# Performance work log

Measured on AMD Instinct MI355X. Metric: run time of the kernel, lower is better.

## Reference

```python
import jax, jax.numpy as jnp
import numpy as np

N, T, CUT = 64, 2, 25.0            # atoms, atom types, cutoff radius
ED = [3, 32, 64, 128]              # embedding MLP dims (input 3)
LD = [384, 256, 256, 128, 3]       # per-atom MLP dims (input 3*E)
P = T * (T + 1) // 2               # number of unordered type pairs
M = 27 * N                         # periodic images


def setup_inputs() -> dict:
    key = jax.random.key(0)
    ks = jax.random.split(key, 16)
    x = jax.random.uniform(ks[0], (N, 3), jnp.float32) * 10.0
    lattice = 10.0 * jnp.eye(3, dtype=jnp.float32)
    atom_types = (jnp.arange(N) % T).astype(jnp.int32)

    def lin(k, shape, fan_in):
        return jax.random.normal(k, shape, jnp.float32) / np.sqrt(fan_in)

    inp = {"x": x, "lattice": lattice}
    for i in range(3):
        inp[f"We{i+1}"] = lin(ks[1 + i], (P, ED[i], ED[i + 1]), ED[i])
        inp[f"be{i+1}"] = jnp.zeros((P, ED[i + 1]), jnp.float32)
    for i in range(4):
        inp[f"Wl{i+1}"] = lin(ks[5 + i], (N, LD[i], LD[i + 1]), LD[i])
        inp[f"bl{i+1}"] = jnp.zeros((N, LD[i + 1]), jnp.float32)
    inp["atom_types"] = atom_types
    return inp


def reference(x, lattice, We1, be1, We2, be2, We3, be3,
              Wl1, bl1, Wl2, bl2, Wl3, bl3, Wl4, bl4, atom_types):
    act = jax.nn.leaky_relu  # slope 0.01, matches nn.LeakyReLU default
    idx = jnp.arange(-1, 2, dtype=x.dtype)
    # (i,j,k) combos in the same loop order as torch (i slowest, k fastest)
    combos = jnp.stack(jnp.meshgrid(idx, idx, idx, indexing="ij"), -1).reshape(27, 3)
    x_ext = (x[None, :, :] + (combos @ lattice)[:, None, :]).reshape(M, 3)  # [M,3]
    # the in-place subtraction in torch telescopes: at step n, x_ext = x_ext0 - x_ext0[n]
    rel = x_ext[None, :, :] - x_ext[:N, None, :]                    # [N,M,3]
    dist = jnp.linalg.norm(rel, axis=-1)                            # [N,M]
    mask = dist <= CUT
    rank = jnp.cumsum(mask, axis=1) - 1
    # torch removes POSITION n of the compacted neighbor list -> rank == n
    keep = (mask & (rank != jnp.arange(N)[:, None])).astype(x.dtype)  # [N,M]

    types_ext = jnp.tile(atom_types, 27)                            # [M]
    lo = jnp.minimum(atom_types[:, None], types_ext[None, :])
    hi = jnp.maximum(atom_types[:, None], types_ext[None, :])
    pid = lo * T - (lo * (lo - 1)) // 2 + (hi - lo)                 # [N,M] pair-type id

    # run all P pair-type embedding MLPs on every candidate edge, then route
    h = act(jnp.einsum("nmi,pio->pnmo", rel, We1) + be1[:, None, None, :])
    h = act(jnp.einsum("pnmi,pio->pnmo", h, We2) + be2[:, None, None, :])
    h = act(jnp.einsum("pnmi,pio->pnmo", h, We3) + be3[:, None, None, :])
    g = h[pid, jnp.arange(N)[:, None], jnp.arange(M)[None, :], :]   # [N,M,E]

    # d_n = g_n^T @ x_n over kept neighbors; row-major flatten of [E,3] -> [3E]
    d = jnp.einsum("nm,nme,nmc->nec", keep, g, rel).reshape(N, -1)  # [N,3E]

    h = act(jnp.einsum("ni,nio->no", d, Wl1) + bl1)
    h = act(jnp.einsum("ni,nio->no", h, Wl2) + bl2)
    h = act(jnp.einsum("ni,nio->no", h, Wl3) + bl3)
    out = jnp.einsum("ni,nio->no", h, Wl4) + bl4                    # [N,3]
    out = out - jnp.mean(out, axis=0, keepdims=True)
    return out.reshape(-1)                                          # [3N]
```

## Files before the change

### kernel.cpp

```cpp
#include <hip/hip_runtime.h>

#define LEAKY(t) ((t) > 0.0f ? (t) : 0.01f*(t))

typedef __attribute__((ext_vector_type(8))) short short8;
typedef __attribute__((ext_vector_type(4))) float floatx4;

static __device__ __forceinline__ short f2bf(float f) {
  unsigned u = __float_as_uint(f);
  u += 0x7FFFu + ((u >> 16) & 1u);
  return (short)(u >> 16);
}

__global__ __launch_bounds__(256) void embed_kernel(
    const float* __restrict__ x, const float* __restrict__ lattice,
    const float* __restrict__ We1, const float* __restrict__ be1,
    const float* __restrict__ We2, const float* __restrict__ be2,
    const float* __restrict__ We3, const float* __restrict__ be3,
    const int* __restrict__ types, float* __restrict__ dpt)
{
  __shared__ __align__(16) unsigned char smem[59392];
  float* W1f = (float*)smem;
  float* b2f = (float*)(smem + 512);
  float* b3f = (float*)(smem + 768);
  short* W2T = (short*)(smem + 1280);
  short* W3T = (short*)(smem + 6400);
  short* h1s = (short*)(smem + 24832);
  short* h2s = (short*)(smem + 36352);
  float* rk4 = (float*)(smem + 57088);

  const int n = blockIdx.x, par = blockIdx.y, chunk = blockIdx.z;
  const int tid = threadIdx.x;

  const int tn = types[n];
  const int tj = types[par];
  const int lo = tn < tj ? tn : tj;
  const int hi = tn < tj ? tj : tn;
  const int p  = lo * 2 - (lo * (lo - 1)) / 2 + (hi - lo);

  if (tid < 96)  W1f[tid] = We1[p*96 + tid];
  if (tid >= 96 && tid < 128) W1f[tid] = be1[p*32 + tid - 96];
  if (tid < 64)  b2f[tid] = be2[p*64 + tid];
  if (tid < 128) b3f[tid] = be3[p*128 + tid];
  for (int idx = tid; idx < 2048; idx += 256) {
    const int i = idx >> 6, o = idx & 63;
    W2T[o*40 + i] = f2bf(We2[p*2048 + idx]);
  }
  for (int idx = tid; idx < 8192; idx += 256) {
    const int i = idx >> 7, o = idx & 127;
    W3T[o*72 + i] = f2bf(We3[p*8192 + idx]);
  }
  __syncthreads();

  if (tid < 144) {
    const int q  = chunk*144 + tid;
    const int c  = q >> 5;
    const int jj = q & 31;
    const int j  = 2*jj + par;
    const float f0 = (float)(c / 9);
    const float f1 = (float)((c / 3) % 3);
    const float f2c = (float)(c % 3);
    const float rel0 = x[j*3+0] - x[n*3+0] + f0*lattice[0] + f1*lattice[3] + f2c*lattice[6];
    const float rel1 = x[j*3+1] - x[n*3+1] + f0*lattice[1] + f1*lattice[4] + f2c*lattice[7];
    const float rel2 = x[j*3+2] - x[n*3+2] + f0*lattice[2] + f1*lattice[5] + f2c*lattice[8];
    const float dist2 = rel0*rel0 + rel1*rel1 + rel2*rel2;
    const int m = c*64 + j;
    const bool keep = (dist2 <= 625.0f) && (m != n);
    const float kf = keep ? 1.0f : 0.0f;
    rk4[tid*4+0] = rel0*kf; rk4[tid*4+1] = rel1*kf;
    rk4[tid*4+2] = rel2*kf; rk4[tid*4+3] = 0.0f;
    #pragma unroll
    for (int o = 0; o < 32; ++o) {
      float v = rel0*W1f[o] + rel1*W1f[32+o] + rel2*W1f[64+o] + W1f[96+o];
      h1s[tid*40 + o] = f2bf(LEAKY(v));
    }
  }
  __syncthreads();

  const int lane = tid & 63, w = tid >> 6;
  const int col = lane & 15, quad = lane >> 4;

  {
    const short8 bfrag = *(const short8*)&W2T[(w*16+col)*40 + quad*8];
    const float bias2 = b2f[w*16+col];
    #pragma unroll
    for (int m = 0; m < 9; ++m) {
      const short8 a = *(const short8*)&h1s[(m*16+col)*40 + quad*8];
      floatx4 acc = {bias2, bias2, bias2, bias2};
      acc = __builtin_amdgcn_mfma_f32_16x16x32_bf16(a, bfrag, acc, 0, 0, 0);
      #pragma unroll
      for (int r = 0; r < 4; ++r) {
        const int pair = m*16 + quad*4 + r;
        h2s[pair*72 + w*16 + col] = f2bf(LEAKY(acc[r]));
      }
    }
  }
  __syncthreads();

  {
    short8 bfrag[2][2];
    float bias3[2];
    #pragma unroll
    for (int nt = 0; nt < 2; ++nt) {
      bias3[nt] = b3f[w*32 + nt*16 + col];
      #pragma unroll
      for (int ks = 0; ks < 2; ++ks)
        bfrag[nt][ks] = *(const short8*)&W3T[(w*32 + nt*16 + col)*72 + ks*32 + quad*8];
    }
    float vacc[2][3] = {{0,0,0},{0,0,0}};
    #pragma unroll
    for (int m = 0; m < 9; ++m) {
      const short8 a0 = *(const short8*)&h2s[(m*16+col)*72 +  0 + quad*8];
      const short8 a1 = *(const short8*)&h2s[(m*16+col)*72 + 32 + quad*8];
      float4 rks[4];
      #pragma unroll
      for (int r = 0; r < 4; ++r)
        rks[r] = *(const float4*)&rk4[(m*16 + quad*4 + r)*4];
      #pragma unroll
      for (int nt = 0; nt < 2; ++nt) {
        floatx4 acc = {bias3[nt], bias3[nt], bias3[nt], bias3[nt]};
        acc = __builtin_amdgcn_mfma_f32_16x16x32_bf16(a0, bfrag[nt][0], acc, 0, 0, 0);
        acc = __builtin_amdgcn_mfma_f32_16x16x32_bf16(a1, bfrag[nt][1], acc, 0, 0, 0);
        #pragma unroll
        for (int r = 0; r < 4; ++r) {
          const float h3 = LEAKY(acc[r]);
          vacc[nt][0] += h3 * rks[r].x;
          vacc[nt][1] += h3 * rks[r].y;
          vacc[nt][2] += h3 * rks[r].z;
        }
      }
    }
    #pragma unroll
    for (int nt = 0; nt < 2; ++nt)
      #pragma unroll
      for (int c = 0; c < 3; ++c) {
        float v = vacc[nt][c];
        v += __shfl_xor(v, 16, 64);
        v += __shfl_xor(v, 32, 64);
        vacc[nt][c] = v;
      }
    if (lane < 32) {
      const int nts = lane >> 4, colw = lane & 15;
      const int o = w*32 + nts*16 + colw;
      #pragma unroll
      for (int c = 0; c < 3; ++c) {
        const float val = nts ? vacc[1][c] : vacc[0][c];
        atomicAdd(&dpt[n*384 + o*3 + c], val);
      }
    }
  }
}

__global__ __launch_bounds__(256) void fit1_kernel(
    const float* __restrict__ d, const float* __restrict__ W,
    const float* __restrict__ b, float* __restrict__ out)
{
  __shared__ float din[384];
  __shared__ floatx4 red[256];
  const int n = blockIdx.x, slice = blockIdx.y, tid = threadIdx.x;
  for (int i = tid; i < 384; i += 256) din[i] = d[n*384 + i];
  __syncthreads();
  const int g = tid & 15, s = tid >> 4;
  const int os = slice*64;
  const float* Wp = W + (size_t)n*98304 + os + 4*g;
  floatx4 acc = {0,0,0,0};
  #pragma unroll 6
  for (int k = 0; k < 24; ++k) {
    const int i = s*24 + k;
    const floatx4 w4 = *(const floatx4*)(Wp + (size_t)i*256);
    acc += din[i] * w4;
  }
  red[tid] = acc;
  __syncthreads();
  #pragma unroll
  for (int off = 128; off >= 16; off >>= 1) {
    if (tid < off) red[tid] += red[tid + off];
    __syncthreads();
  }
  if (tid < 16) {
    const floatx4 v = red[tid];
    const int o = os + 4*tid;
    const float4 bb = *(const float4*)&b[n*256 + o];
    float4 r;
    r.x = LEAKY(v[0] + bb.x); r.y = LEAKY(v[1] + bb.y);
    r.z = LEAKY(v[2] + bb.z); r.w = LEAKY(v[3] + bb.w);
    *(float4*)&out[n*256 + o] = r;
  }
}

__global__ __launch_bounds__(256) void fit2_kernel(
    const float* __restrict__ in, const float* __restrict__ W,
    const float* __restrict__ b, float* __restrict__ out)
{
  __shared__ float din[256];
  __shared__ floatx4 red[256];
  const int n = blockIdx.x, slice = blockIdx.y, tid = threadIdx.x;
  din[tid] = in[n*256 + tid];
  __syncthreads();
  const int g = tid & 15, s = tid >> 4;
  const int os = slice*64;
  const float* Wp = W + (size_t)n*65536 + os + 4*g;
  floatx4 acc = {0,0,0,0};
  #pragma unroll 8
  for (int k = 0; k < 16; ++k) {
    const int i = s*16 + k;
    const floatx4 w4 = *(const floatx4*)(Wp + (size_t)i*256);
    acc += din[i] * w4;
  }
  red[tid] = acc;
  __syncthreads();
  #pragma unroll
  for (int off = 128; off >= 16; off >>= 1) {
    if (tid < off) red[tid] += red[tid + off];
    __syncthreads();
  }
  if (tid < 16) {
    const floatx4 v = red[tid];
    const int o = os + 4*tid;
    const float4 bb = *(const float4*)&b[n*256 + o];
    float4 r;
    r.x = LEAKY(v[0] + bb.x); r.y = LEAKY(v[1] + bb.y);
    r.z = LEAKY(v[2] + bb.z); r.w = LEAKY(v[3] + bb.w);
    *(float4*)&out[n*256 + o] = r;
  }
}

__global__ __launch_bounds__(256) void fit3_kernel(
    const float* __restrict__ in, const float* __restrict__ W,
    const float* __restrict__ b, float* __restrict__ out)
{
  __shared__ float din[256];
  __shared__ floatx4 red[256];
  const int n = blockIdx.x, slice = blockIdx.y, tid = threadIdx.x;
  din[tid] = in[n*256 + tid];
  __syncthreads();
  const int g = tid & 7, s = tid >> 3;
  const int os = slice*32;
  const float* Wp = W + (size_t)n*32768 + os + 4*g;
  floatx4 acc = {0,0,0,0};
  #pragma unroll 8
  for (int k = 0; k < 8; ++k) {
    const int i = s*8 + k;
    const floatx4 w4 = *(const floatx4*)(Wp + (size_t)i*128);
    acc += din[i] * w4;
  }
  red[tid] = acc;
  __syncthreads();
  #pragma unroll
  for (int off = 128; off >= 8; off >>= 1) {
    if (tid < off) red[tid] += red[tid + off];
    __syncthreads();
  }
  if (tid < 8) {
    const floatx4 v = red[tid];
    const int o = os + 4*tid;
    const float4 bb = *(const float4*)&b[n*128 + o];
    float4 r;
    r.x = LEAKY(v[0] + bb.x); r.y = LEAKY(v[1] + bb.y);
    r.z = LEAKY(v[2] + bb.z); r.w = LEAKY(v[3] + bb.w);
    *(float4*)&out[n*128 + o] = r;
  }
}

__global__ __launch_bounds__(256) void fit4_kernel(
    const float* __restrict__ h3, const float* __restrict__ W,
    const float* __restrict__ b, float* __restrict__ out)
{
  __shared__ float part[256 * 3];
  __shared__ float pre[192];
  __shared__ float meanv[3];
  const int tid = threadIdx.x;
  const int n = tid >> 2, q = tid & 3;
  const float* Wn = W + (size_t)n * 384;
  const float* h  = h3 + n * 128;
  float a0 = 0.f, a1 = 0.f, a2 = 0.f;
  for (int k = 0; k < 32; ++k) {
    const int i = q * 32 + k;
    const float hv = h[i];
    a0 += hv * Wn[i*3 + 0];
    a1 += hv * Wn[i*3 + 1];
    a2 += hv * Wn[i*3 + 2];
  }
  part[tid*3+0] = a0; part[tid*3+1] = a1; part[tid*3+2] = a2;
  __syncthreads();
  if (tid < 192) {
    const int nn = tid / 3, o = tid % 3;
    float t = part[(nn*4+0)*3+o] + part[(nn*4+1)*3+o]
            + part[(nn*4+2)*3+o] + part[(nn*4+3)*3+o] + b[tid];
    pre[tid] = t;
  }
  __syncthreads();
  if (tid < 3) {
    float s = 0.f;
    for (int nn = 0; nn < 64; ++nn) s += pre[nn*3 + tid];
    meanv[tid] = s * (1.0f / 64.0f);
  }
  __syncthreads();
  if (tid < 192) out[tid] = pre[tid] - meanv[tid % 3];
}

extern "C" void kernel_launch(void* const* d_in, const int* in_sizes, int n_in,
                              void* d_out, int out_size, void* d_ws, size_t ws_size,
                              hipStream_t stream) {
  const float* x       = (const float*)d_in[0];
  const float* lattice = (const float*)d_in[1];
  const float* We1 = (const float*)d_in[2];
  const float* be1 = (const float*)d_in[3];
  const float* We2 = (const float*)d_in[4];
  const float* be2 = (const float*)d_in[5];
  const float* We3 = (const float*)d_in[6];
  const float* be3 = (const float*)d_in[7];
  const float* Wl1 = (const float*)d_in[8];
  const float* bl1 = (const float*)d_in[9];
  const float* Wl2 = (const float*)d_in[10];
  const float* bl2 = (const float*)d_in[11];
  const float* Wl3 = (const float*)d_in[12];
  const float* bl3 = (const float*)d_in[13];
  const float* Wl4 = (const float*)d_in[14];
  const float* bl4 = (const float*)d_in[15];
  const int*   types = (const int*)d_in[16];

  float* w   = (float*)d_ws;
  float* dpt = w;
  float* h1f = w + 24576;
  float* h2f = h1f + 16384;
  float* h3f = h2f + 16384;

  hipMemsetAsync(dpt, 0, 64*384*sizeof(float), stream);
  embed_kernel<<<dim3(64, 2, 6), 256, 0, stream>>>(
      x, lattice, We1, be1, We2, be2, We3, be3, types, dpt);
  fit1_kernel<<<dim3(64, 4), 256, 0, stream>>>(dpt, Wl1, bl1, h1f);
  fit2_kernel<<<dim3(64, 4), 256, 0, stream>>>(h1f, Wl2, bl2, h2f);
  fit3_kernel<<<dim3(64, 4), 256, 0, stream>>>(h2f, Wl3, bl3, h3f);
  fit4_kernel<<<1, 256, 0, stream>>>(h3f, Wl4, bl4, (float*)d_out);
}
```

Measured before the change: 150.7 us.

## Pre-transpose embedding weights, drop atomics, fuse fitting layers 2-4

A new prep kernel converts and transposes the embedding weights to bf16 once per call, so each embed block copies them with vector loads instead of transposing them itself. The embed output goes to per-block partial slots that fit1 sums, which removes the memset and the atomic adds. The layer-1 activation is computed from interleaved float4 weights and stored as packed short8. Fit layers 2-4 and the mean subtraction are merged into one kernel that uses a last-block counter, cutting three launches. In exchange the fused fit kernel runs on only 64 blocks, and it adds an extra launch plus more workspace.

```diff
diff --git a/kernel.cpp b/kernel.cpp
--- a/kernel.cpp
+++ b/kernel.cpp
@@ -11,15 +11,38 @@
   return (short)(u >> 16);
 }
 
+
+__global__ __launch_bounds__(256) void prep_kernel(
+    const float* __restrict__ We1, const float* __restrict__ be1,
+    const float* __restrict__ We2, const float* __restrict__ We3,
+    float* __restrict__ g_W1v, short* __restrict__ g_WT,
+    unsigned int* __restrict__ cnt)
+{
+  const int gt = blockIdx.x * 256 + threadIdx.x;
+  const int GS = gridDim.x * 256;
+  if (gt == 0) *cnt = 0;
+  for (int idx = gt; idx < 3 * 128; idx += GS) {
+    const int p = idx >> 7, r = idx & 127, o = r >> 2, c = r & 3;
+    g_W1v[idx] = (c < 3) ? We1[p * 96 + c * 32 + o] : be1[p * 32 + o];
+  }
+  for (int idx = gt; idx < 3 * 2560; idx += GS) {
+    const int p = idx / 2560, r = idx % 2560, o = r / 40, i = r % 40;
+    g_WT[p * 11776 + o * 40 + i] = (i < 32) ? f2bf(We2[p * 2048 + i * 64 + o]) : (short)0;
+  }
+  for (int idx = gt; idx < 3 * 9216; idx += GS) {
+    const int p = idx / 9216, r = idx % 9216, o = r / 72, i = r % 72;
+    g_WT[p * 11776 + 2560 + o * 72 + i] = (i < 64) ? f2bf(We3[p * 8192 + i * 128 + o]) : (short)0;
+  }
+}
+
 __global__ __launch_bounds__(256) void embed_kernel(
     const float* __restrict__ x, const float* __restrict__ lattice,
-    const float* __restrict__ We1, const float* __restrict__ be1,
-    const float* __restrict__ We2, const float* __restrict__ be2,
-    const float* __restrict__ We3, const float* __restrict__ be3,
+    const float* __restrict__ g_W1v, const short* __restrict__ g_WT,
+    const float* __restrict__ be2, const float* __restrict__ be3,
     const int* __restrict__ types, float* __restrict__ dpt)
 {
   __shared__ __align__(16) unsigned char smem[59392];
-  float* W1f = (float*)smem;
+  float* W1v = (float*)smem;
   float* b2f = (float*)(smem + 512);
   float* b3f = (float*)(smem + 768);
   short* W2T = (short*)(smem + 1280);
@@ -37,25 +60,25 @@
   const int hi = tn < tj ? tj : tn;
   const int p  = lo * 2 - (lo * (lo - 1)) / 2 + (hi - lo);
 
-  if (tid < 96)  W1f[tid] = We1[p*96 + tid];
-  if (tid >= 96 && tid < 128) W1f[tid] = be1[p*32 + tid - 96];
-  if (tid < 64)  b2f[tid] = be2[p*64 + tid];
-  if (tid < 128) b3f[tid] = be3[p*128 + tid];
-  for (int idx = tid; idx < 2048; idx += 256) {
-    const int i = idx >> 6, o = idx & 63;
-    W2T[o*40 + i] = f2bf(We2[p*2048 + idx]);
-  }
-  for (int idx = tid; idx < 8192; idx += 256) {
-    const int i = idx >> 7, o = idx & 127;
-    W3T[o*72 + i] = f2bf(We3[p*8192 + idx]);
+  if (tid < 32) ((float4*)W1v)[tid] = ((const float4*)(g_W1v + p * 128))[tid];
+  if (tid < 64)  b2f[tid] = be2[p * 64 + tid];
+  if (tid < 128) b3f[tid] = be3[p * 128 + tid];
+  {
+    const short8* src = (const short8*)(g_WT + p * 11776);
+    short8* dst = (short8*)W2T;
+    #pragma unroll
+    for (int k = 0; k < 6; ++k) {
+      const int idx = tid + k * 256;
+      if (idx < 1472) dst[idx] = src[idx];
+    }
   }
   __syncthreads();
 
   if (tid < 144) {
-    const int q  = chunk*144 + tid;
+    const int q  = chunk * 144 + tid;
     const int c  = q >> 5;
     const int jj = q & 31;
-    const int j  = 2*jj + par;
+    const int j  = 2 * jj + par;
     const float f0 = (float)(c / 9);
     const float f1 = (float)((c / 3) % 3);
     const float f2c = (float)(c % 3);
@@ -63,15 +86,22 @@
     const float rel1 = x[j*3+1] - x[n*3+1] + f0*lattice[1] + f1*lattice[4] + f2c*lattice[7];
     const float rel2 = x[j*3+2] - x[n*3+2] + f0*lattice[2] + f1*lattice[5] + f2c*lattice[8];
     const float dist2 = rel0*rel0 + rel1*rel1 + rel2*rel2;
-    const int m = c*64 + j;
+    const int m = c * 64 + j;
     const bool keep = (dist2 <= 625.0f) && (m != n);
     const float kf = keep ? 1.0f : 0.0f;
     rk4[tid*4+0] = rel0*kf; rk4[tid*4+1] = rel1*kf;
     rk4[tid*4+2] = rel2*kf; rk4[tid*4+3] = 0.0f;
-    #pragma unroll
-    for (int o = 0; o < 32; ++o) {
-      float v = rel0*W1f[o] + rel1*W1f[32+o] + rel2*W1f[64+o] + W1f[96+o];
-      h1s[tid*40 + o] = f2bf(LEAKY(v));
+    const float4* W1v4 = (const float4*)W1v;
+    #pragma unroll
+    for (int g = 0; g < 4; ++g) {
+      short8 pk;
+      #pragma unroll
+      for (int u = 0; u < 8; ++u) {
+        const float4 wv = W1v4[g*8 + u];
+        const float v = rel0*wv.x + rel1*wv.y + rel2*wv.z + wv.w;
+        pk[u] = f2bf(LEAKY(v));
+      }
+      *(short8*)&h1s[tid*40 + g*8] = pk;
     }
   }
   __syncthreads();
@@ -141,33 +171,37 @@
     if (lane < 32) {
       const int nts = lane >> 4, colw = lane & 15;
       const int o = w*32 + nts*16 + colw;
-      #pragma unroll
-      for (int c = 0; c < 3; ++c) {
-        const float val = nts ? vacc[1][c] : vacc[0][c];
-        atomicAdd(&dpt[n*384 + o*3 + c], val);
-      }
+      float* dst = dpt + ((size_t)(n*12) + par*6 + chunk) * 384 + o*3;
+      dst[0] = nts ? vacc[1][0] : vacc[0][0];
+      dst[1] = nts ? vacc[1][1] : vacc[0][1];
+      dst[2] = nts ? vacc[1][2] : vacc[0][2];
     }
   }
 }
 
 __global__ __launch_bounds__(256) void fit1_kernel(
-    const float* __restrict__ d, const float* __restrict__ W,
+    const float* __restrict__ dpt, const float* __restrict__ W,
     const float* __restrict__ b, float* __restrict__ out)
 {
   __shared__ float din[384];
   __shared__ floatx4 red[256];
   const int n = blockIdx.x, slice = blockIdx.y, tid = threadIdx.x;
-  for (int i = tid; i < 384; i += 256) din[i] = d[n*384 + i];
+  for (int i = tid; i < 384; i += 256) {
+    const float* dp = dpt + (size_t)n * 4608 + i;
+    float s = 0.f;
+    #pragma unroll
+    for (int k = 0; k < 12; ++k) s += dp[k * 384];
+    din[i] = s;
+  }
   __syncthreads();
   const int g = tid & 15, s = tid >> 4;
-  const int os = slice*64;
-  const float* Wp = W + (size_t)n*98304 + os + 4*g;
-  floatx4 acc = {0,0,0,0};
+  const int os = slice * 64;
+  const float* Wp = W + (size_t)n * 98304 + os + 4 * g;
+  floatx4 acc = {0, 0, 0, 0};
   #pragma unroll 6
   for (int k = 0; k < 24; ++k) {
-    const int i = s*24 + k;
-    const floatx4 w4 = *(const floatx4*)(Wp + (size_t)i*256);
-    acc += din[i] * w4;
+    const int i = s * 24 + k;
+    acc += din[i] * *(const floatx4*)(Wp + (size_t)i * 256);
   }
   red[tid] = acc;
   __syncthreads();
@@ -178,124 +212,121 @@
   }
   if (tid < 16) {
     const floatx4 v = red[tid];
-    const int o = os + 4*tid;
-    const float4 bb = *(const float4*)&b[n*256 + o];
+    const int o = os + 4 * tid;
+    const float4 bb = *(const float4*)&b[n * 256 + o];
     float4 r;
     r.x = LEAKY(v[0] + bb.x); r.y = LEAKY(v[1] + bb.y);
     r.z = LEAKY(v[2] + bb.z); r.w = LEAKY(v[3] + bb.w);
-    *(float4*)&out[n*256 + o] = r;
-  }
-}
-
-__global__ __launch_bounds__(256) void fit2_kernel(
-    const float* __restrict__ in, const float* __restrict__ W,
-    const float* __restrict__ b, float* __restrict__ out)
+    *(float4*)&out[n * 256 + o] = r;
+  }
+}
+
+__global__ __launch_bounds__(512) void fit234_kernel(
+    const float* __restrict__ h1f,
+    const float* __restrict__ Wl2, const float* __restrict__ bl2,
+    const float* __restrict__ Wl3, const float* __restrict__ bl3,
+    const float* __restrict__ Wl4, const float* __restrict__ bl4,
+    float* __restrict__ pre_g, unsigned int* __restrict__ cnt,
+    float* __restrict__ out)
 {
-  __shared__ float din[256];
-  __shared__ floatx4 red[256];
-  const int n = blockIdx.x, slice = blockIdx.y, tid = threadIdx.x;
-  din[tid] = in[n*256 + tid];
-  __syncthreads();
-  const int g = tid & 15, s = tid >> 4;
-  const int os = slice*64;
-  const float* Wp = W + (size_t)n*65536 + os + 4*g;
-  floatx4 acc = {0,0,0,0};
-  #pragma unroll 8
-  for (int k = 0; k < 16; ++k) {
-    const int i = s*16 + k;
-    const floatx4 w4 = *(const floatx4*)(Wp + (size_t)i*256);
-    acc += din[i] * w4;
-  }
-  red[tid] = acc;
+  __shared__ float h[256];
+  __shared__ floatx4 red[512];
+  __shared__ float h3s[128];
+  __shared__ float pre_s[192];
+  __shared__ int amlast;
+  const int n = blockIdx.x, tid = threadIdx.x;
+
+  if (tid < 256) h[tid] = h1f[n * 256 + tid];
+  __syncthreads();
+
+  {
+    const int o4 = tid & 63, s = tid >> 6;
+    const float* Wp = Wl2 + (size_t)n * 65536 + 4 * o4;
+    floatx4 acc = {0, 0, 0, 0};
+    #pragma unroll 8
+    for (int k = 0; k < 32; ++k) {
+      const int i = s * 32 + k;
+      acc += h[i] * *(const floatx4*)(Wp + (size_t)i * 256);
+    }
+    red[tid] = acc;
+  }
+  __syncthreads();
+  if (tid < 64) {
+    floatx4 a = red[tid];
+    #pragma unroll
+    for (int s = 1; s < 8; ++s) a += red[tid + s * 64];
+    const float4 bb = *(const float4*)&bl2[n * 256 + 4 * tid];
+    h[4*tid+0] = LEAKY(a[0] + bb.x);
+    h[4*tid+1] = LEAKY(a[1] + bb.y);
+    h[4*tid+2] = LEAKY(a[2] + bb.z);
+    h[4*tid+3] = LEAKY(a[3] + bb.w);
+  }
+  __syncthreads();
+
+  {
+    const int o4 = tid & 31, s = tid >> 5;
+    const float* Wp = Wl3 + (size_t)n * 32768 + 4 * o4;
+    floatx4 acc = {0, 0, 0, 0};
+    #pragma unroll 8
+    for (int k = 0; k < 16; ++k) {
+      const int i = s * 16 + k;
+      acc += h[i] * *(const floatx4*)(Wp + (size_t)i * 128);
+    }
+    red[tid] = acc;
+  }
+  __syncthreads();
+  if (tid < 32) {
+    floatx4 a = red[tid];
+    #pragma unroll
+    for (int s = 1; s < 16; ++s) a += red[tid + s * 32];
+    const float4 bb = *(const float4*)&bl3[n * 128 + 4 * tid];
+    h3s[4*tid+0] = LEAKY(a[0] + bb.x);
+    h3s[4*tid+1] = LEAKY(a[1] + bb.y);
+    h3s[4*tid+2] = LEAKY(a[2] + bb.z);
+    h3s[4*tid+3] = LEAKY(a[3] + bb.w);
+  }
+  __syncthreads();
+
+  if (tid < 128) {
+    const float hv = h3s[tid];
+    floatx4 v;
+    v[0] = hv * Wl4[(size_t)n * 384 + tid * 3 + 0];
+    v[1] = hv * Wl4[(size_t)n * 384 + tid * 3 + 1];
+    v[2] = hv * Wl4[(size_t)n * 384 + tid * 3 + 2];
+    v[3] = 0.f;
+    red[tid] = v;
+  }
   __syncthreads();
   #pragma unroll
-  for (int off = 128; off >= 16; off >>= 1) {
+  for (int off = 64; off >= 1; off >>= 1) {
     if (tid < off) red[tid] += red[tid + off];
     __syncthreads();
   }
-  if (tid < 16) {
-    const floatx4 v = red[tid];
-    const int o = os + 4*tid;
-    const float4 bb = *(const float4*)&b[n*256 + o];
-    float4 r;
-    r.x = LEAKY(v[0] + bb.x); r.y = LEAKY(v[1] + bb.y);
-    r.z = LEAKY(v[2] + bb.z); r.w = LEAKY(v[3] + bb.w);
-    *(float4*)&out[n*256 + o] = r;
-  }
-}
-
-__global__ __launch_bounds__(256) void fit3_kernel(
-    const float* __restrict__ in, const float* __restrict__ W,
-    const float* __restrict__ b, float* __restrict__ out)
-{
-  __shared__ float din[256];
-  __shared__ floatx4 red[256];
-  const int n = blockIdx.x, slice = blockIdx.y, tid = threadIdx.x;
-  din[tid] = in[n*256 + tid];
-  __syncthreads();
-  const int g = tid & 7, s = tid >> 3;
-  const int os = slice*32;
-  const float* Wp = W + (size_t)n*32768 + os + 4*g;
-  floatx4 acc = {0,0,0,0};
-  #pragma unroll 8
-  for (int k = 0; k < 8; ++k) {
-    const int i = s*8 + k;
-    const floatx4 w4 = *(const floatx4*)(Wp + (size_t)i*128);
-    acc += din[i] * w4;
-  }
-  red[tid] = acc;
-  __syncthreads();
-  #pragma unroll
-  for (int off = 128; off >= 8; off >>= 1) {
-    if (tid < off) red[tid] += red[tid + off];
+  if (tid < 3) {
+    const float pre = red[0][tid] + bl4[n * 3 + tid];
+    __hip_atomic_store(&pre_g[n * 3 + tid], pre, __ATOMIC_RELAXED,
+                       __HIP_MEMORY_SCOPE_AGENT);
+  }
+  __threadfence();
+  if (tid == 0) {
+    const unsigned old = __hip_atomic_fetch_add(cnt, 1u, __ATOMIC_ACQ_REL,
+                                                __HIP_MEMORY_SCOPE_AGENT);
+    amlast = (old == 63u);
+  }
+  __syncthreads();
+  if (amlast) {
+    if (tid < 192)
+      pre_s[tid] = __hip_atomic_load(&pre_g[tid], __ATOMIC_RELAXED,
+                                     __HIP_MEMORY_SCOPE_AGENT);
     __syncthreads();
-  }
-  if (tid < 8) {
-    const floatx4 v = red[tid];
-    const int o = os + 4*tid;
-    const float4 bb = *(const float4*)&b[n*128 + o];
-    float4 r;
-    r.x = LEAKY(v[0] + bb.x); r.y = LEAKY(v[1] + bb.y);
-    r.z = LEAKY(v[2] + bb.z); r.w = LEAKY(v[3] + bb.w);
-    *(float4*)&out[n*128 + o] = r;
-  }
-}
-
-__global__ __launch_bounds__(256) void fit4_kernel(
-    const float* __restrict__ h3, const float* __restrict__ W,
-    const float* __restrict__ b, float* __restrict__ out)
-{
-  __shared__ float part[256 * 3];
-  __shared__ float pre[192];
-  __shared__ float meanv[3];
-  const int tid = threadIdx.x;
-  const int n = tid >> 2, q = tid & 3;
-  const float* Wn = W + (size_t)n * 384;
-  const float* h  = h3 + n * 128;
-  float a0 = 0.f, a1 = 0.f, a2 = 0.f;
-  for (int k = 0; k < 32; ++k) {
-    const int i = q * 32 + k;
-    const float hv = h[i];
-    a0 += hv * Wn[i*3 + 0];
-    a1 += hv * Wn[i*3 + 1];
-    a2 += hv * Wn[i*3 + 2];
-  }
-  part[tid*3+0] = a0; part[tid*3+1] = a1; part[tid*3+2] = a2;
-  __syncthreads();
-  if (tid < 192) {
-    const int nn = tid / 3, o = tid % 3;
-    float t = part[(nn*4+0)*3+o] + part[(nn*4+1)*3+o]
-            + part[(nn*4+2)*3+o] + part[(nn*4+3)*3+o] + b[tid];
-    pre[tid] = t;
-  }
-  __syncthreads();
-  if (tid < 3) {
-    float s = 0.f;
-    for (int nn = 0; nn < 64; ++nn) s += pre[nn*3 + tid];
-    meanv[tid] = s * (1.0f / 64.0f);
-  }
-  __syncthreads();
-  if (tid < 192) out[tid] = pre[tid] - meanv[tid % 3];
+    if (tid < 3) {
+      float s = 0.f;
+      for (int nn = 0; nn < 64; ++nn) s += pre_s[nn * 3 + tid];
+      h3s[tid] = s * (1.0f / 64.0f);
+    }
+    __syncthreads();
+    if (tid < 192) out[tid] = pre_s[tid] - h3s[tid % 3];
+  }
 }
 
 extern "C" void kernel_launch(void* const* d_in, const int* in_sizes, int n_in,
@@ -319,17 +350,18 @@
   const float* bl4 = (const float*)d_in[15];
   const int*   types = (const int*)d_in[16];
 
-  float* w   = (float*)d_ws;
-  float* dpt = w;
-  float* h1f = w + 24576;
-  float* h2f = h1f + 16384;
-  float* h3f = h2f + 16384;
-
-  hipMemsetAsync(dpt, 0, 64*384*sizeof(float), stream);
+  float* wsf = (float*)d_ws;
+  float*        dpt   = wsf;
+  float*        h1f   = wsf + 294912;
+  float*        pre_g = wsf + 311296;
+  unsigned int* cnt   = (unsigned int*)(wsf + 311488);
+  float*        g_W1v = wsf + 311492;
+  short*        g_WT  = (short*)(wsf + 311876);
+
+  prep_kernel<<<64, 256, 0, stream>>>(We1, be1, We2, We3, g_W1v, g_WT, cnt);
   embed_kernel<<<dim3(64, 2, 6), 256, 0, stream>>>(
-      x, lattice, We1, be1, We2, be2, We3, be3, types, dpt);
+      x, lattice, g_W1v, g_WT, be2, be3, types, dpt);
   fit1_kernel<<<dim3(64, 4), 256, 0, stream>>>(dpt, Wl1, bl1, h1f);
-  fit2_kernel<<<dim3(64, 4), 256, 0, stream>>>(h1f, Wl2, bl2, h2f);
-  fit3_kernel<<<dim3(64, 4), 256, 0, stream>>>(h2f, Wl3, bl3, h3f);
-  fit4_kernel<<<1, 256, 0, stream>>>(h3f, Wl4, bl4, (float*)d_out);
-}
+  fit234_kernel<<<64, 512, 0, stream>>>(h1f, Wl2, bl2, Wl3, bl3, Wl4, bl4,
+                                        pre_g, cnt, (float*)d_out);
+}
```

After: 147.2 us. -2.3%, faster.

## Prepack embedding weights, MFMA first layer, fuse fit3/fit4, widen fit grids

Applied to the files above, without the earlier changes.

A new prep kernel converts the embedding weights to bf16 in MFMA fragment order once and also zeroes the accumulator and a counter, which replaces the memset. The embed kernel then loads weight fragments straight into registers instead of transposing them into LDS in every block, and computes layer 1 with MFMA. The fit kernels run on twice as many blocks with smaller output slices. fit3 and fit4 are merged through a last-block-done atomic counter, removing one launch at the cost of fence and atomic overhead.

```diff
diff --git a/kernel.cpp b/kernel.cpp
--- a/kernel.cpp
+++ b/kernel.cpp
@@ -11,25 +11,72 @@
   return (short)(u >> 16);
 }
 
-__global__ __launch_bounds__(256) void embed_kernel(
+
+__global__ __launch_bounds__(256) void prep_kernel(
+    const float* __restrict__ We1, const float* __restrict__ be1,
+    const float* __restrict__ We2, const float* __restrict__ We3,
+    short* __restrict__ g_WT, float* __restrict__ d,
+    unsigned int* __restrict__ cnt)
+{
+  const int gt = blockIdx.x * 256 + threadIdx.x;
+  const int GS = gridDim.x * 256;
+  if (gt == 0) *cnt = 0;
+  for (int i = gt; i < 6144; i += GS) {
+    const float4 z = {0.f, 0.f, 0.f, 0.f};
+    ((float4*)d)[i] = z;
+  }
+  for (int it = gt; it < 4224; it += GS) {
+    short8 v;
+    if (it < 384) {
+      const int p = it >> 7, r = it & 127, ot = (r >> 6) & 1, ln = r & 63;
+      const int col = ln & 15, quad = ln >> 4, o = ot * 16 + col;
+      #pragma unroll
+      for (int j = 0; j < 8; ++j) {
+        const int k = quad * 8 + j;
+        float f = 0.0f;
+        if (k < 3) f = We1[p * 96 + k * 32 + o];
+        else if (k == 3) f = be1[p * 32 + o];
+        v[j] = f2bf(f);
+      }
+    } else if (it < 1152) {
+      const int t = it - 384;
+      const int p = t >> 8, r = t & 255, ot = r >> 6, ln = r & 63;
+      const int col = ln & 15, quad = ln >> 4, o = ot * 16 + col;
+      #pragma unroll
+      for (int j = 0; j < 8; ++j) {
+        const int k = quad * 8 + j;
+        v[j] = f2bf(We2[p * 2048 + k * 64 + o]);
+      }
+    } else {
+      const int t = it - 1152;
+      const int p = t >> 10, r = t & 1023, ot = r >> 7, rr = r & 127;
+      const int ks = rr >> 6, ln = rr & 63;
+      const int col = ln & 15, quad = ln >> 4, o = ot * 16 + col;
+      #pragma unroll
+      for (int j = 0; j < 8; ++j) {
+        const int k = ks * 32 + quad * 8 + j;
+        v[j] = f2bf(We3[p * 8192 + k * 128 + o]);
+      }
+    }
+    *(short8*)(g_WT + it * 8) = v;
+  }
+}
+
+__global__ __launch_bounds__(256, 4) void embed_kernel(
     const float* __restrict__ x, const float* __restrict__ lattice,
-    const float* __restrict__ We1, const float* __restrict__ be1,
-    const float* __restrict__ We2, const float* __restrict__ be2,
-    const float* __restrict__ We3, const float* __restrict__ be3,
-    const int* __restrict__ types, float* __restrict__ dpt)
-{
-  __shared__ __align__(16) unsigned char smem[59392];
-  float* W1f = (float*)smem;
-  float* b2f = (float*)(smem + 512);
-  float* b3f = (float*)(smem + 768);
-  short* W2T = (short*)(smem + 1280);
-  short* W3T = (short*)(smem + 6400);
-  short* h1s = (short*)(smem + 24832);
-  short* h2s = (short*)(smem + 36352);
-  float* rk4 = (float*)(smem + 57088);
+    const short* __restrict__ g_WT,
+    const float* __restrict__ be2, const float* __restrict__ be3,
+    const int* __restrict__ types, float* __restrict__ d)
+{
+  __shared__ __align__(16) float rel4[144 * 4];
+  __shared__ __align__(16) float rk4[144 * 4];
+  __shared__ __align__(16) short h1s[144 * 40];
+  __shared__ __align__(16) short h2s[144 * 72];
 
   const int n = blockIdx.x, par = blockIdx.y, chunk = blockIdx.z;
   const int tid = threadIdx.x;
+  const int lane = tid & 63, w = tid >> 6;
+  const int col = lane & 15, quad = lane >> 4;
 
   const int tn = types[n];
   const int tj = types[par];
@@ -37,25 +84,30 @@
   const int hi = tn < tj ? tj : tn;
   const int p  = lo * 2 - (lo * (lo - 1)) / 2 + (hi - lo);
 
-  if (tid < 96)  W1f[tid] = We1[p*96 + tid];
-  if (tid >= 96 && tid < 128) W1f[tid] = be1[p*32 + tid - 96];
-  if (tid < 64)  b2f[tid] = be2[p*64 + tid];
-  if (tid < 128) b3f[tid] = be3[p*128 + tid];
-  for (int idx = tid; idx < 2048; idx += 256) {
-    const int i = idx >> 6, o = idx & 63;
-    W2T[o*40 + i] = f2bf(We2[p*2048 + idx]);
-  }
-  for (int idx = tid; idx < 8192; idx += 256) {
-    const int i = idx >> 7, o = idx & 127;
-    W3T[o*72 + i] = f2bf(We3[p*8192 + idx]);
-  }
-  __syncthreads();
+  const short8* WT8 = (const short8*)g_WT;
+  const short8 w1b0 = WT8[(p * 2 + 0) * 64 + lane];
+  const short8 w1b1 = WT8[(p * 2 + 1) * 64 + lane];
+  short8 w2b[4];
+  #pragma unroll
+  for (int ot = 0; ot < 4; ++ot) w2b[ot] = WT8[384 + (p * 4 + ot) * 64 + lane];
+  short8 w3b[2][2];
+  #pragma unroll
+  for (int nt = 0; nt < 2; ++nt)
+    #pragma unroll
+    for (int ks = 0; ks < 2; ++ks)
+      w3b[nt][ks] = WT8[1152 + ((p * 8 + 2 * w + nt) * 2 + ks) * 64 + lane];
+  float bias2[4];
+  #pragma unroll
+  for (int ot = 0; ot < 4; ++ot) bias2[ot] = be2[p * 64 + ot * 16 + col];
+  float bias3[2];
+  #pragma unroll
+  for (int nt = 0; nt < 2; ++nt) bias3[nt] = be3[p * 128 + w * 32 + nt * 16 + col];
 
   if (tid < 144) {
-    const int q  = chunk*144 + tid;
+    const int q  = chunk * 144 + tid;
     const int c  = q >> 5;
     const int jj = q & 31;
-    const int j  = 2*jj + par;
+    const int j  = 2 * jj + par;
     const float f0 = (float)(c / 9);
     const float f1 = (float)((c / 3) % 3);
     const float f2c = (float)(c % 3);
@@ -63,90 +115,87 @@
     const float rel1 = x[j*3+1] - x[n*3+1] + f0*lattice[1] + f1*lattice[4] + f2c*lattice[7];
     const float rel2 = x[j*3+2] - x[n*3+2] + f0*lattice[2] + f1*lattice[5] + f2c*lattice[8];
     const float dist2 = rel0*rel0 + rel1*rel1 + rel2*rel2;
-    const int m = c*64 + j;
+    const int m = c * 64 + j;
     const bool keep = (dist2 <= 625.0f) && (m != n);
     const float kf = keep ? 1.0f : 0.0f;
+    rel4[tid*4+0] = rel0; rel4[tid*4+1] = rel1;
+    rel4[tid*4+2] = rel2; rel4[tid*4+3] = 1.0f;
     rk4[tid*4+0] = rel0*kf; rk4[tid*4+1] = rel1*kf;
     rk4[tid*4+2] = rel2*kf; rk4[tid*4+3] = 0.0f;
-    #pragma unroll
-    for (int o = 0; o < 32; ++o) {
-      float v = rel0*W1f[o] + rel1*W1f[32+o] + rel2*W1f[64+o] + W1f[96+o];
-      h1s[tid*40 + o] = f2bf(LEAKY(v));
-    }
-  }
-  __syncthreads();
-
-  const int lane = tid & 63, w = tid >> 6;
-  const int col = lane & 15, quad = lane >> 4;
-
-  {
-    const short8 bfrag = *(const short8*)&W2T[(w*16+col)*40 + quad*8];
-    const float bias2 = b2f[w*16+col];
-    #pragma unroll
-    for (int m = 0; m < 9; ++m) {
-      const short8 a = *(const short8*)&h1s[(m*16+col)*40 + quad*8];
-      floatx4 acc = {bias2, bias2, bias2, bias2};
-      acc = __builtin_amdgcn_mfma_f32_16x16x32_bf16(a, bfrag, acc, 0, 0, 0);
+  }
+  __syncthreads();
+
+  for (int mt = w; mt < 9; mt += 4) {
+    const float4 r4 = *(const float4*)&rel4[(mt*16 + col) * 4];
+    short8 a = {0, 0, 0, 0, 0, 0, 0, 0};
+    if (quad == 0) {
+      a[0] = f2bf(r4.x); a[1] = f2bf(r4.y); a[2] = f2bf(r4.z);
+      a[3] = (short)0x3F80;
+    }
+    const floatx4 z = {0.f, 0.f, 0.f, 0.f};
+    const floatx4 c0 = __builtin_amdgcn_mfma_f32_16x16x32_bf16(a, w1b0, z, 0, 0, 0);
+    const floatx4 c1 = __builtin_amdgcn_mfma_f32_16x16x32_bf16(a, w1b1, z, 0, 0, 0);
+    #pragma unroll
+    for (int r = 0; r < 4; ++r) {
+      const int pair = mt*16 + quad*4 + r;
+      h1s[pair*40 +      col] = f2bf(LEAKY(c0[r]));
+      h1s[pair*40 + 16 + col] = f2bf(LEAKY(c1[r]));
+    }
+  }
+  __syncthreads();
+
+  for (int mt = w; mt < 9; mt += 4) {
+    const short8 a = *(const short8*)&h1s[(mt*16 + col) * 40 + quad*8];
+    #pragma unroll
+    for (int ot = 0; ot < 4; ++ot) {
+      floatx4 acc = {bias2[ot], bias2[ot], bias2[ot], bias2[ot]};
+      acc = __builtin_amdgcn_mfma_f32_16x16x32_bf16(a, w2b[ot], acc, 0, 0, 0);
       #pragma unroll
       for (int r = 0; r < 4; ++r) {
-        const int pair = m*16 + quad*4 + r;
-        h2s[pair*72 + w*16 + col] = f2bf(LEAKY(acc[r]));
-      }
-    }
-  }
-  __syncthreads();
-
-  {
-    short8 bfrag[2][2];
-    float bias3[2];
+        const int pair = mt*16 + quad*4 + r;
+        h2s[pair*72 + ot*16 + col] = f2bf(LEAKY(acc[r]));
+      }
+    }
+  }
+  __syncthreads();
+
+  float vacc[2][3] = {{0,0,0},{0,0,0}};
+  for (int mt = 0; mt < 9; ++mt) {
+    const short8 a0 = *(const short8*)&h2s[(mt*16 + col) * 72 +      quad*8];
+    const short8 a1 = *(const short8*)&h2s[(mt*16 + col) * 72 + 32 + quad*8];
+    float4 rks[4];
+    #pragma unroll
+    for (int r = 0; r < 4; ++r)
+      rks[r] = *(const float4*)&rk4[(mt*16 + quad*4 + r) * 4];
     #pragma unroll
     for (int nt = 0; nt < 2; ++nt) {
-      bias3[nt] = b3f[w*32 + nt*16 + col];
-      #pragma unroll
-      for (int ks = 0; ks < 2; ++ks)
-        bfrag[nt][ks] = *(const short8*)&W3T[(w*32 + nt*16 + col)*72 + ks*32 + quad*8];
-    }
-    float vacc[2][3] = {{0,0,0},{0,0,0}};
-    #pragma unroll
-    for (int m = 0; m < 9; ++m) {
-      const short8 a0 = *(const short8*)&h2s[(m*16+col)*72 +  0 + quad*8];
-      const short8 a1 = *(const short8*)&h2s[(m*16+col)*72 + 32 + quad*8];
-      float4 rks[4];
-      #pragma unroll
-      for (int r = 0; r < 4; ++r)
-        rks[r] = *(const float4*)&rk4[(m*16 + quad*4 + r)*4];
-      #pragma unroll
-      for (int nt = 0; nt < 2; ++nt) {
-        floatx4 acc = {bias3[nt], bias3[nt], bias3[nt], bias3[nt]};
-        acc = __builtin_amdgcn_mfma_f32_16x16x32_bf16(a0, bfrag[nt][0], acc, 0, 0, 0);
-        acc = __builtin_amdgcn_mfma_f32_16x16x32_bf16(a1, bfrag[nt][1], acc, 0, 0, 0);
-        #pragma unroll
-        for (int r = 0; r < 4; ++r) {
-          const float h3 = LEAKY(acc[r]);
-          vacc[nt][0] += h3 * rks[r].x;
-          vacc[nt][1] += h3 * rks[r].y;
-          vacc[nt][2] += h3 * rks[r].z;
-        }
-      }
-    }
-    #pragma unroll
-    for (int nt = 0; nt < 2; ++nt)
-      #pragma unroll
-      for (int c = 0; c < 3; ++c) {
-        float v = vacc[nt][c];
-        v += __shfl_xor(v, 16, 64);
-        v += __shfl_xor(v, 32, 64);
-        vacc[nt][c] = v;
-      }
-    if (lane < 32) {
-      const int nts = lane >> 4, colw = lane & 15;
-      const int o = w*32 + nts*16 + colw;
-      #pragma unroll
-      for (int c = 0; c < 3; ++c) {
-        const float val = nts ? vacc[1][c] : vacc[0][c];
-        atomicAdd(&dpt[n*384 + o*3 + c], val);
-      }
-    }
+      floatx4 acc = {bias3[nt], bias3[nt], bias3[nt], bias3[nt]};
+      acc = __builtin_amdgcn_mfma_f32_16x16x32_bf16(a0, w3b[nt][0], acc, 0, 0, 0);
+      acc = __builtin_amdgcn_mfma_f32_16x16x32_bf16(a1, w3b[nt][1], acc, 0, 0, 0);
+      #pragma unroll
+      for (int r = 0; r < 4; ++r) {
+        const float h3 = LEAKY(acc[r]);
+        vacc[nt][0] += h3 * rks[r].x;
+        vacc[nt][1] += h3 * rks[r].y;
+        vacc[nt][2] += h3 * rks[r].z;
+      }
+    }
+  }
+  #pragma unroll
+  for (int nt = 0; nt < 2; ++nt)
+    #pragma unroll
+    for (int c = 0; c < 3; ++c) {
+      float v = vacc[nt][c];
+      v += __shfl_xor(v, 16, 64);
+      v += __shfl_xor(v, 32, 64);
+      vacc[nt][c] = v;
+    }
+  if (lane < 32) {
+    const int nts = lane >> 4, colw = lane & 15;
+    const int o = w*32 + nts*16 + colw;
+    #pragma unroll
+    for (int c = 0; c < 3; ++c)
+      atomicAdd(&d[n*384 + o*3 + c], nts ? vacc[1][c] : vacc[0][c]);
   }
 }
 
@@ -156,29 +205,27 @@
 {
   __shared__ float din[384];
   __shared__ floatx4 red[256];
-  const int n = blockIdx.x, slice = blockIdx.y, tid = threadIdx.x;
+  const int n = blockIdx.x, os = blockIdx.y * 32, tid = threadIdx.x;
   for (int i = tid; i < 384; i += 256) din[i] = d[n*384 + i];
   __syncthreads();
-  const int g = tid & 15, s = tid >> 4;
-  const int os = slice*64;
-  const float* Wp = W + (size_t)n*98304 + os + 4*g;
-  floatx4 acc = {0,0,0,0};
-  #pragma unroll 6
-  for (int k = 0; k < 24; ++k) {
-    const int i = s*24 + k;
-    const floatx4 w4 = *(const floatx4*)(Wp + (size_t)i*256);
-    acc += din[i] * w4;
+  const int g = tid & 7, s = tid >> 3;
+  const float* Wp = W + (size_t)n * 98304 + os + 4 * g;
+  floatx4 acc = {0, 0, 0, 0};
+  #pragma unroll
+  for (int k = 0; k < 12; ++k) {
+    const int i = s * 12 + k;
+    acc += din[i] * *(const floatx4*)(Wp + (size_t)i * 256);
   }
   red[tid] = acc;
   __syncthreads();
   #pragma unroll
-  for (int off = 128; off >= 16; off >>= 1) {
+  for (int off = 128; off >= 8; off >>= 1) {
     if (tid < off) red[tid] += red[tid + off];
     __syncthreads();
   }
-  if (tid < 16) {
+  if (tid < 8) {
     const floatx4 v = red[tid];
-    const int o = os + 4*tid;
+    const int o = os + 4 * tid;
     const float4 bb = *(const float4*)&b[n*256 + o];
     float4 r;
     r.x = LEAKY(v[0] + bb.x); r.y = LEAKY(v[1] + bb.y);
@@ -193,29 +240,27 @@
 {
   __shared__ float din[256];
   __shared__ floatx4 red[256];
-  const int n = blockIdx.x, slice = blockIdx.y, tid = threadIdx.x;
+  const int n = blockIdx.x, os = blockIdx.y * 32, tid = threadIdx.x;
   din[tid] = in[n*256 + tid];
   __syncthreads();
-  const int g = tid & 15, s = tid >> 4;
-  const int os = slice*64;
-  const float* Wp = W + (size_t)n*65536 + os + 4*g;
-  floatx4 acc = {0,0,0,0};
-  #pragma unroll 8
-  for (int k = 0; k < 16; ++k) {
-    const int i = s*16 + k;
-    const floatx4 w4 = *(const floatx4*)(Wp + (size_t)i*256);
-    acc += din[i] * w4;
+  const int g = tid & 7, s = tid >> 3;
+  const float* Wp = W + (size_t)n * 65536 + os + 4 * g;
+  floatx4 acc = {0, 0, 0, 0};
+  #pragma unroll
+  for (int k = 0; k < 8; ++k) {
+    const int i = s * 8 + k;
+    acc += din[i] * *(const floatx4*)(Wp + (size_t)i * 256);
   }
   red[tid] = acc;
   __syncthreads();
   #pragma unroll
-  for (int off = 128; off >= 16; off >>= 1) {
+  for (int off = 128; off >= 8; off >>= 1) {
     if (tid < off) red[tid] += red[tid + off];
     __syncthreads();
   }
-  if (tid < 16) {
+  if (tid < 8) {
     const floatx4 v = red[tid];
-    const int o = os + 4*tid;
+    const int o = os + 4 * tid;
     const float4 bb = *(const float4*)&b[n*256 + o];
     float4 r;
     r.x = LEAKY(v[0] + bb.x); r.y = LEAKY(v[1] + bb.y);
@@ -224,78 +269,81 @@
   }
 }
 
-__global__ __launch_bounds__(256) void fit3_kernel(
+__global__ __launch_bounds__(256) void fit34_kernel(
     const float* __restrict__ in, const float* __restrict__ W,
-    const float* __restrict__ b, float* __restrict__ out)
+    const float* __restrict__ b,
+    const float* __restrict__ Wl4, const float* __restrict__ bl4,
+    float* __restrict__ h3f, unsigned int* __restrict__ cnt,
+    float* __restrict__ out)
 {
   __shared__ float din[256];
   __shared__ floatx4 red[256];
-  const int n = blockIdx.x, slice = blockIdx.y, tid = threadIdx.x;
+  __shared__ float fin[256];
+  __shared__ int amlast;
+  const int n = blockIdx.x, os = blockIdx.y * 16, tid = threadIdx.x;
   din[tid] = in[n*256 + tid];
   __syncthreads();
-  const int g = tid & 7, s = tid >> 3;
-  const int os = slice*32;
-  const float* Wp = W + (size_t)n*32768 + os + 4*g;
-  floatx4 acc = {0,0,0,0};
-  #pragma unroll 8
-  for (int k = 0; k < 8; ++k) {
-    const int i = s*8 + k;
-    const floatx4 w4 = *(const floatx4*)(Wp + (size_t)i*128);
-    acc += din[i] * w4;
+  const int g = tid & 3, s = tid >> 2;
+  const float* Wp = W + (size_t)n * 32768 + os + 4 * g;
+  floatx4 acc = {0, 0, 0, 0};
+  #pragma unroll
+  for (int k = 0; k < 4; ++k) {
+    const int i = s * 4 + k;
+    acc += din[i] * *(const floatx4*)(Wp + (size_t)i * 128);
   }
   red[tid] = acc;
   __syncthreads();
   #pragma unroll
-  for (int off = 128; off >= 8; off >>= 1) {
+  for (int off = 128; off >= 4; off >>= 1) {
     if (tid < off) red[tid] += red[tid + off];
     __syncthreads();
   }
-  if (tid < 8) {
+  if (tid < 4) {
     const floatx4 v = red[tid];
-    const int o = os + 4*tid;
+    const int o = os + 4 * tid;
     const float4 bb = *(const float4*)&b[n*128 + o];
-    float4 r;
-    r.x = LEAKY(v[0] + bb.x); r.y = LEAKY(v[1] + bb.y);
-    r.z = LEAKY(v[2] + bb.z); r.w = LEAKY(v[3] + bb.w);
-    *(float4*)&out[n*128 + o] = r;
-  }
-}
-
-__global__ __launch_bounds__(256) void fit4_kernel(
-    const float* __restrict__ h3, const float* __restrict__ W,
-    const float* __restrict__ b, float* __restrict__ out)
-{
-  __shared__ float part[256 * 3];
-  __shared__ float pre[192];
-  __shared__ float meanv[3];
-  const int tid = threadIdx.x;
-  const int n = tid >> 2, q = tid & 3;
-  const float* Wn = W + (size_t)n * 384;
-  const float* h  = h3 + n * 128;
-  float a0 = 0.f, a1 = 0.f, a2 = 0.f;
-  for (int k = 0; k < 32; ++k) {
-    const int i = q * 32 + k;
-    const float hv = h[i];
-    a0 += hv * Wn[i*3 + 0];
-    a1 += hv * Wn[i*3 + 1];
-    a2 += hv * Wn[i*3 + 2];
-  }
-  part[tid*3+0] = a0; part[tid*3+1] = a1; part[tid*3+2] = a2;
-  __syncthreads();
-  if (tid < 192) {
-    const int nn = tid / 3, o = tid % 3;
-    float t = part[(nn*4+0)*3+o] + part[(nn*4+1)*3+o]
-            + part[(nn*4+2)*3+o] + part[(nn*4+3)*3+o] + b[tid];
-    pre[tid] = t;
-  }
-  __syncthreads();
-  if (tid < 3) {
-    float s = 0.f;
-    for (int nn = 0; nn < 64; ++nn) s += pre[nn*3 + tid];
-    meanv[tid] = s * (1.0f / 64.0f);
-  }
-  __syncthreads();
-  if (tid < 192) out[tid] = pre[tid] - meanv[tid % 3];
+    #pragma unroll
+    for (int u = 0; u < 4; ++u)
+      __hip_atomic_store(&h3f[n*128 + o + u],
+                         LEAKY(v[u] + ((const float*)&bb)[u]),
+                         __ATOMIC_RELAXED, __HIP_MEMORY_SCOPE_AGENT);
+  }
+  __threadfence();
+  if (tid == 0) {
+    const unsigned old = __hip_atomic_fetch_add(cnt, 1u, __ATOMIC_ACQ_REL,
+                                                __HIP_MEMORY_SCOPE_AGENT);
+    amlast = (old == 511u);
+  }
+  __syncthreads();
+  if (amlast) {
+    float* part = (float*)red;
+    const int nn = tid >> 2, q = tid & 3;
+    const float* Wn = Wl4 + (size_t)nn * 384;
+    float a0 = 0.f, a1 = 0.f, a2 = 0.f;
+    for (int k = 0; k < 32; ++k) {
+      const int i = q * 32 + k;
+      const float hv = __hip_atomic_load(&h3f[nn*128 + i], __ATOMIC_RELAXED,
+                                         __HIP_MEMORY_SCOPE_AGENT);
+      a0 += hv * Wn[i*3 + 0];
+      a1 += hv * Wn[i*3 + 1];
+      a2 += hv * Wn[i*3 + 2];
+    }
+    part[tid*3+0] = a0; part[tid*3+1] = a1; part[tid*3+2] = a2;
+    __syncthreads();
+    if (tid < 192) {
+      const int a = tid / 3, o = tid % 3;
+      fin[tid] = part[(a*4+0)*3+o] + part[(a*4+1)*3+o]
+               + part[(a*4+2)*3+o] + part[(a*4+3)*3+o] + bl4[tid];
+    }
+    __syncthreads();
+    if (tid < 3) {
+      float sm = 0.f;
+      for (int a = 0; a < 64; ++a) sm += fin[a*3 + tid];
+      fin[200 + tid] = sm * (1.0f / 64.0f);
+    }
+    __syncthreads();
+    if (tid < 192) out[tid] = fin[tid] - fin[200 + (tid % 3)];
+  }
 }
 
 extern "C" void kernel_launch(void* const* d_in, const int* in_sizes, int n_in,
@@ -319,17 +367,19 @@
   const float* bl4 = (const float*)d_in[15];
   const int*   types = (const int*)d_in[16];
 
-  float* w   = (float*)d_ws;
-  float* dpt = w;
-  float* h1f = w + 24576;
-  float* h2f = h1f + 16384;
-  float* h3f = h2f + 16384;
-
-  hipMemsetAsync(dpt, 0, 64*384*sizeof(float), stream);
+  float* wsf = (float*)d_ws;
+  float*        d    = wsf;
+  float*        h1f  = wsf + 24576;
+  float*        h2f  = wsf + 40960;
+  float*        h3f  = wsf + 57344;
+  unsigned int* cnt  = (unsigned int*)(wsf + 65536);
+  short*        g_WT = (short*)(wsf + 65540);
+
+  prep_kernel<<<32, 256, 0, stream>>>(We1, be1, We2, We3, g_WT, d, cnt);
   embed_kernel<<<dim3(64, 2, 6), 256, 0, stream>>>(
-      x, lattice, We1, be1, We2, be2, We3, be3, types, dpt);
-  fit1_kernel<<<dim3(64, 4), 256, 0, stream>>>(dpt, Wl1, bl1, h1f);
-  fit2_kernel<<<dim3(64, 4), 256, 0, stream>>>(h1f, Wl2, bl2, h2f);
-  fit3_kernel<<<dim3(64, 4), 256, 0, stream>>>(h2f, Wl3, bl3, h3f);
-  fit4_kernel<<<1, 256, 0, stream>>>(h3f, Wl4, bl4, (float*)d_out);
-}
+      x, lattice, g_WT, be2, be3, types, d);
+  fit1_kernel<<<dim3(64, 8), 256, 0, stream>>>(d, Wl1, bl1, h1f);
+  fit2_kernel<<<dim3(64, 8), 256, 0, stream>>>(h1f, Wl2, bl2, h2f);
+  fit34_kernel<<<dim3(64, 8), 256, 0, stream>>>(h2f, Wl3, bl3, Wl4, bl4,
+                                                h3f, cnt, (float*)d_out);
+}
```

Measured after the change: 180.4 us. 19.7% more time.
